# Optimization experiments

Measured on AMD Instinct MI355X. Metric: run time of the kernel, lower is better.

## Reference

```python
import jax, jax.numpy as jnp
import numpy as np

N_QUBITS = 8
INPUT_DIM = 256
SEQ_LEN = 256
BATCH = 512


def qgate(theta, x):
    # Closed-form expectation of the PennyLane circuit:
    #   RX(x_i) then RY(theta_i) on each wire (from |0>), then CNOT chain 0->1->...->n-1,
    #   measure <Z_k>.  Single-wire <Z_j> = cos(x_j) * cos(theta_j); CNOT chain maps
    #   Z_k -> Z_0 Z_1 ... Z_k in the Heisenberg picture, so on the product state
    #   <Z_k> = prod_{j<=k} cos(x_j) cos(theta_j).
    # x: (B, n_wires), theta: (n_wires,)
    return jnp.cumprod(jnp.cos(x) * jnp.cos(theta), axis=-1)


def setup_inputs() -> dict:
    key = jax.random.key(0)
    ks = jax.random.split(key, 14)
    d_in = INPUT_DIM + N_QUBITS  # concat([x, hx]) -> 264
    lin_scale = 1.0 / np.sqrt(d_in)
    inp = {
        "inputs": jax.random.normal(ks[0], (SEQ_LEN, BATCH, INPUT_DIM), dtype=jnp.float32),
        "Wf": jax.random.normal(ks[1], (N_QUBITS, d_in), dtype=jnp.float32) * lin_scale,
        "bf": jax.random.normal(ks[2], (N_QUBITS,), dtype=jnp.float32) * lin_scale,
        "Wi": jax.random.normal(ks[3], (N_QUBITS, d_in), dtype=jnp.float32) * lin_scale,
        "bi": jax.random.normal(ks[4], (N_QUBITS,), dtype=jnp.float32) * lin_scale,
        "Wu": jax.random.normal(ks[5], (N_QUBITS, d_in), dtype=jnp.float32) * lin_scale,
        "bu": jax.random.normal(ks[6], (N_QUBITS,), dtype=jnp.float32) * lin_scale,
        "Wo": jax.random.normal(ks[7], (N_QUBITS, d_in), dtype=jnp.float32) * lin_scale,
        "bo": jax.random.normal(ks[8], (N_QUBITS,), dtype=jnp.float32) * lin_scale,
        "pf": jax.random.normal(ks[9], (N_QUBITS,), dtype=jnp.float32),
        "pi_": jax.random.normal(ks[10], (N_QUBITS,), dtype=jnp.float32),
        "pu": jax.random.normal(ks[11], (N_QUBITS,), dtype=jnp.float32),
        "po": jax.random.normal(ks[12], (N_QUBITS,), dtype=jnp.float32),
    }
    return inp


def reference(inputs, Wf, bf, Wi, bi, Wu, bu, Wo, bo, pf, pi_, pu, po):
    B = inputs.shape[1]
    H = pf.shape[0]  # hidden_dim == n_qubits

    def step(carry, x):
        hx, cx = carry
        comb = jnp.concatenate([x, hx], axis=1)  # (B, input_dim + H)
        f = jax.nn.sigmoid(qgate(pf, comb @ Wf.T + bf))
        i = jax.nn.sigmoid(qgate(pi_, comb @ Wi.T + bi))
        g = jnp.tanh(qgate(pu, comb @ Wu.T + bu))
        o = jax.nn.sigmoid(qgate(po, comb @ Wo.T + bo))
        cx = f * cx + i * g
        hx = o * jnp.tanh(cx)
        return (hx, cx), hx

    init = (jnp.zeros((B, H), dtype=inputs.dtype), jnp.zeros((B, H), dtype=inputs.dtype))
    (hx, cx), stacked = jax.lax.scan(step, init, inputs)
    return stacked, hx, cx
```

## Files before the change

### kernel.cpp

```cpp
#include <hip/hip_runtime.h>
#include <hip/hip_bf16.h>


#define SEQ   256
#define BATCH 512
#define DIN   256
#define NROWS (SEQ * BATCH)
#define DCOMB 264
#define ZTSTR 514
#define HLSTR 260

typedef __attribute__((ext_vector_type(8))) short short8;
typedef __attribute__((ext_vector_type(4))) float f32x4;
typedef __attribute__((ext_vector_type(2))) float f32x2;

__device__ __forceinline__ short f2bf(float f) {
    union { __hip_bfloat16 h; short s; } u;
    u.h = __float2bfloat16(f);
    return u.s;
}
__device__ __forceinline__ float bf2f(short s) {
    union { short s; __hip_bfloat16 h; } u;
    u.s = s;
    return __bfloat162float(u.h);
}

__device__ __forceinline__ short8 pack8(float4 a, float4 b) {
    union { short8 s8; int i[4]; } u;
    union { __hip_bfloat162 h; int i; } v;
    v.h = __float22bfloat162_rn(make_float2(a.x, a.y)); u.i[0] = v.i;
    v.h = __float22bfloat162_rn(make_float2(a.z, a.w)); u.i[1] = v.i;
    v.h = __float22bfloat162_rn(make_float2(b.x, b.y)); u.i[2] = v.i;
    v.h = __float22bfloat162_rn(make_float2(b.z, b.w)); u.i[3] = v.i;
    return u.s8;
}

#define DPP_ROR(V, S) \
    __int_as_float(__builtin_amdgcn_update_dpp(__float_as_int(V), __float_as_int(V), 0x120 | (S), 0xF, 0xF, false))
#define QP(V, CTRL) \
    __int_as_float(__builtin_amdgcn_update_dpp(__float_as_int(V), __float_as_int(V), (CTRL), 0xF, 0xF, false))
#define PSTG2(A, D) { \
    float s0_ = __int_as_float(__builtin_amdgcn_update_dpp(one_i, __float_as_int(A.x), 0x110 | (D), 0xF, 0xF, false)); \
    float s1_ = __int_as_float(__builtin_amdgcn_update_dpp(one_i, __float_as_int(A.y), 0x110 | (D), 0xF, 0xF, false)); \
    A *= (f32x2){s0_, s1_}; }

__device__ __forceinline__ void scan_body8(
    int T0, const float* __restrict__ zrow, float* __restrict__ hlrow,
    bool writer, f32x4 (&ZC)[4], f32x4 (&ZN)[4],
    float& hx, float& cx,
    const f32x2 (&wp)[8], const f32x2 cth,
    const f32x2 k0, const f32x2 k1, const f32x2 k2, const f32x2 k3,
    const f32x2 k4, const int one_i)
{
    #pragma unroll
    for (int j = 0; j < 4; ++j)
        ZN[j] = *(const f32x4*)&zrow[(T0 + 8) * 2 + j * 4];

    float hxh[8];
    #pragma unroll
    for (int u = 0; u < 8; ++u) {
        const f32x2 z2 = (f32x2){ ZC[u >> 1][(u & 1) * 2],
                                  ZC[u >> 1][(u & 1) * 2 + 1] };

        const float h0 = hx;
        const float h1 = DPP_ROR(hx, 2),  h2 = DPP_ROR(hx, 4);
        const float h3 = DPP_ROR(hx, 6),  h4 = DPP_ROR(hx, 8);
        const float h5 = DPP_ROR(hx, 10), h6 = DPP_ROR(hx, 12);
        const float h7 = DPP_ROR(hx, 14);

        f32x2 e0 = (f32x2){h0, h0} * wp[0] + (f32x2){h1, h1} * wp[1];
        f32x2 e1 = (f32x2){h2, h2} * wp[2] + (f32x2){h3, h3} * wp[3];
        f32x2 e2 = (f32x2){h4, h4} * wp[4] + (f32x2){h5, h5} * wp[5];
        f32x2 e3 = (f32x2){h6, h6} * wp[6] + (f32x2){h7, h7} * wp[7];
        const f32x2 p = ((z2 + e0) + (e1 + e2)) + e3;

        f32x2 A = (f32x2){__cosf(p.x), __cosf(p.y)} * cth;
        PSTG2(A, 2) PSTG2(A, 4) PSTG2(A, 8)

        const f32x2 t2 = A * A;
        f32x2 rr = k3 + t2 * k4;
        rr = k2 + t2 * rr;
        rr = k1 + t2 * rr;
        const f32x2 P = k0 + A * rr;

        const float f_all = QP(P.x, 0xA0);
        const float u_all = QP(P.x, 0xF5);
        const float i_all = QP(P.y, 0xA0);
        const float o_all = QP(P.y, 0xF5);

        cx = fmaf(f_all, cx, i_all * u_all);

        const float tq  = cx * cx;
        const float num = cx * fmaf(tq, fmaf(tq, 1.0f, 105.0f), 945.0f);
        const float den = fmaf(tq, fmaf(tq, 15.0f, 420.0f), 945.0f);
        const float tc  = num * __builtin_amdgcn_rcpf(den);

        hx = o_all * tc;
        hxh[u] = hx;
    }

    if (writer) {
        *(f32x4*)&hlrow[T0]     = (f32x4){hxh[0], hxh[1], hxh[2], hxh[3]};
        *(f32x4*)&hlrow[T0 + 4] = (f32x4){hxh[4], hxh[5], hxh[6], hxh[7]};
    }
}

__global__ __launch_bounds__(512, 2) void qlstm_fused(
    const float* __restrict__ X,
    const float* __restrict__ Wf, const float* __restrict__ Wi,
    const float* __restrict__ Wu, const float* __restrict__ Wo,
    const float* __restrict__ bfv, const float* __restrict__ biv,
    const float* __restrict__ buv, const float* __restrict__ bov,
    const float* __restrict__ pf, const float* __restrict__ pi_,
    const float* __restrict__ pu, const float* __restrict__ po,
    float* __restrict__ out)
{
    __shared__ short8 Wl[2048];
    __shared__ float Zt[32 * ZTSTR + 16];
    __shared__ float Hl2[16 * HLSTR];

    const int tx  = threadIdx.x;
    const int l   = tx & 63;
    const int wid = tx >> 6;
    const int lm  = l & 15;
    const int lk  = l >> 4;
    const int B0  = blockIdx.x;

    const float* Wg[4] = {Wf, Wi, Wu, Wo};
    const float* Bg[4] = {bfv, biv, buv, bov};

    #pragma unroll
    for (int e = 0; e < 4; ++e) {
        const int ent  = tx + e * 512;
        const int lane = ent & 63;
        const int ks   = (ent >> 6) & 7;
        const int hl   = (ent >> 9) & 1;
        const int nt   = (ent >> 10) & 1;
        const int elm  = lane & 15, elk = lane >> 4;
        const int c    = nt * 16 + elm;
        const float* wrow = Wg[c & 3] + (c >> 2) * DCOMB + ks * 32 + elk * 8;
        short8 fr;
        #pragma unroll
        for (int j = 0; j < 8; ++j) {
            const float v = wrow[j];
            const short h16 = f2bf(v);
            fr[j] = hl ? f2bf(v - bf2f(h16)) : h16;
        }
        Wl[ent] = fr;
    }

    float bias0, bias1;
    { const int c0 = lm;      bias0 = Bg[c0 & 3][c0 >> 2];
      const int c1 = 16 + lm; bias1 = Bg[c1 & 3][c1 >> 2]; }

    __syncthreads();

    #pragma unroll
    for (int p = 0; p < 4; ++p) {
        const int r0 = p * 128 + wid * 16;
        const int r  = r0 + lm;
        const float* xbase =
            X + ((long)(r >> 1) * BATCH + B0 * 2 + (r & 1)) * DIN + lk * 8;

        float4 xv[16];
        #pragma unroll
        for (int i = 0; i < 16; ++i)
            xv[i] = *(const float4*)(xbase + (i >> 1) * 32 + (i & 1) * 4);

        f32x4 acc0 = (f32x4){bias0, bias0, bias0, bias0};
        f32x4 acc1 = (f32x4){bias1, bias1, bias1, bias1};
        #pragma unroll
        for (int ks = 0; ks < 8; ++ks) {
            const short8 a = pack8(xv[2 * ks], xv[2 * ks + 1]);
            acc0 = __builtin_amdgcn_mfma_f32_16x16x32_bf16(a, Wl[ks * 64 + l],        acc0, 0, 0, 0);
            acc0 = __builtin_amdgcn_mfma_f32_16x16x32_bf16(a, Wl[(8  + ks) * 64 + l], acc0, 0, 0, 0);
            acc1 = __builtin_amdgcn_mfma_f32_16x16x32_bf16(a, Wl[(16 + ks) * 64 + l], acc1, 0, 0, 0);
            acc1 = __builtin_amdgcn_mfma_f32_16x16x32_bf16(a, Wl[(24 + ks) * 64 + l], acc1, 0, 0, 0);
        }

        #pragma unroll
        for (int rr = 0; rr < 4; ++rr) {
            const int rw = r0 + lk * 4 + rr;
            const int tt = rw >> 1, blw = rw & 1;
            Zt[(blw * 16 + (lm >> 1)) * ZTSTR + tt * 2 + (lm & 1)]     = acc0[rr];
            Zt[(blw * 16 + 8 + (lm >> 1)) * ZTSTR + tt * 2 + (lm & 1)] = acc1[rr];
        }
    }
    __syncthreads();

    if (tx < 64) {
        const int q   = tx & 15;
        const int kq  = q >> 1;
        const int hi  = q & 1;
        const int bl  = (tx >> 4) & 1;
        const int b   = B0 * 2 + bl;
        const int oidx = b * 8 + kq;
        const int woff = kq * DCOMB + DIN;

        const float* WgA = hi ? Wu : Wf;
        const float* WgB = hi ? Wo : Wi;
        f32x2 wp[8];
        #pragma unroll
        for (int s = 0; s < 8; ++s) {
            const int j = (kq - s) & 7;
            wp[s] = (f32x2){WgA[woff + j], WgB[woff + j]};
        }
        const f32x2 cth = (f32x2){__cosf((hi ? pu : pf)[kq]),
                                  __cosf((hi ? po : pi_)[kq])};

        const float SK1 = 0.25f, SK2 = -0.0208333333f, SK3 = 0.0020833333f,
                    SK4 = -0.00021082f;
        const f32x2 k0 = (f32x2){hi ? 0.0f : 0.5f, 0.5f};
        const f32x2 k1 = (f32x2){hi ? 0.9999016f : SK1, SK1};
        const f32x2 k2 = (f32x2){hi ? -0.3310485f : SK2, SK2};
        const f32x2 k3 = (f32x2){hi ? 0.1204423f : SK3, SK3};
        const f32x2 k4 = (f32x2){hi ? -0.0277012f : SK4, SK4};

        const int one_i = __float_as_int(1.0f);

        float hx = 0.0f, cx = 0.0f;
        const float* __restrict__ zrow = &Zt[(bl * 16 + q) * ZTSTR];
        float* __restrict__ hlrow = &Hl2[(bl * 8 + kq) * HLSTR];
        const bool writer = (hi == 0) && (tx < 32);

        f32x4 zbA[4], zbB[4];
        #pragma unroll
        for (int j = 0; j < 4; ++j) zbA[j] = *(const f32x4*)&zrow[j * 4];

        for (int t0 = 0; t0 < SEQ; t0 += 16) {
            scan_body8(t0,     zrow, hlrow, writer, zbA, zbB, hx, cx,
                       wp, cth, k0, k1, k2, k3, k4, one_i);
            scan_body8(t0 + 8, zrow, hlrow, writer, zbB, zbA, hx, cx,
                       wp, cth, k0, k1, k2, k3, k4, one_i);
        }

        if (hi == 0 && tx < 32) {
            out[NROWS * 8 + oidx]        = hx;
            out[NROWS * 8 + 4096 + oidx] = cx;
        }
    }
    __syncthreads();

    {
        const int f0 = tx * 8;
        const int t  = f0 >> 4;
        const int c0 = f0 & 15;
        float4 v0, v1;
        v0.x = Hl2[(c0 + 0) * HLSTR + t];
        v0.y = Hl2[(c0 + 1) * HLSTR + t];
        v0.z = Hl2[(c0 + 2) * HLSTR + t];
        v0.w = Hl2[(c0 + 3) * HLSTR + t];
        v1.x = Hl2[(c0 + 4) * HLSTR + t];
        v1.y = Hl2[(c0 + 5) * HLSTR + t];
        v1.z = Hl2[(c0 + 6) * HLSTR + t];
        v1.w = Hl2[(c0 + 7) * HLSTR + t];
        float4* dst = (float4*)(out + (long)t * (BATCH * 8) + B0 * 16 + c0);
        dst[0] = v0;
        dst[1] = v1;
    }
}

extern "C" void kernel_launch(void* const* d_in, const int* in_sizes, int n_in,
                              void* d_out, int out_size, void* d_ws, size_t ws_size,
                              hipStream_t stream) {
    const float* X   = (const float*)d_in[0];
    const float* Wf  = (const float*)d_in[1];
    const float* bfv = (const float*)d_in[2];
    const float* Wi  = (const float*)d_in[3];
    const float* biv = (const float*)d_in[4];
    const float* Wu  = (const float*)d_in[5];
    const float* buv = (const float*)d_in[6];
    const float* Wo  = (const float*)d_in[7];
    const float* bov = (const float*)d_in[8];
    const float* pf  = (const float*)d_in[9];
    const float* pi_ = (const float*)d_in[10];
    const float* pu  = (const float*)d_in[11];
    const float* po  = (const float*)d_in[12];
    float* out = (float*)d_out;
    (void)d_ws; (void)ws_size;

    qlstm_fused<<<BATCH / 2, 512, 0, stream>>>(
        X, Wf, Wi, Wu, Wo, bfv, biv, buv, bov, pf, pi_, pu, po, out);
}
```

Measured before the change: 249.9 us.

## Overlap input projection GEMM with recurrent scan via double-buffered chunks

The fused kernel previously computed the full input projection for all 256 timesteps into shared memory before one wave ran the sequential recurrence. It now splits the sequence into 64-step chunks: waves 1-4 compute the next chunk's MFMA projection into one of two shared buffers while wave 0 scans the previous chunk. The intent is to hide the projection and global loads behind the latency-bound scan, and the smaller chunk buffers shrink shared memory. In exchange it adds a block barrier per chunk, leaves waves 5-7 idle, and lowers launch bounds to one block per CU, which may reduce occupancy and latency hiding across blocks.

```diff
diff --git a/kernel.cpp b/kernel.cpp
--- a/kernel.cpp
+++ b/kernel.cpp
@@ -7,7 +7,10 @@
 #define DIN   256
 #define NROWS (SEQ * BATCH)
 #define DCOMB 264
-#define ZTSTR 514
+#define CHT   64
+#define NCH   (SEQ / CHT)
+#define ZBSTR 130
+#define ZBUFSZ (32 * ZBSTR + 16)
 #define HLSTR 260
 
 typedef __attribute__((ext_vector_type(8))) short short8;
@@ -45,8 +48,9 @@
     A *= (f32x2){s0_, s1_}; }
 
 __device__ __forceinline__ void scan_body8(
-    int T0, const float* __restrict__ zrow, float* __restrict__ hlrow,
-    bool writer, f32x4 (&ZC)[4], f32x4 (&ZN)[4],
+    int T0L, int T0G, const float* __restrict__ zrow,
+    float* __restrict__ hlrow, bool writer,
+    f32x4 (&ZC)[4], f32x4 (&ZN)[4],
     float& hx, float& cx,
     const f32x2 (&wp)[8], const f32x2 cth,
     const f32x2 k0, const f32x2 k1, const f32x2 k2, const f32x2 k3,
@@ -54,7 +58,7 @@
 {
     #pragma unroll
     for (int j = 0; j < 4; ++j)
-        ZN[j] = *(const f32x4*)&zrow[(T0 + 8) * 2 + j * 4];
+        ZN[j] = *(const f32x4*)&zrow[(T0L + 8) * 2 + j * 4];
 
     float hxh[8];
     #pragma unroll
@@ -100,12 +104,12 @@
     }
 
     if (writer) {
-        *(f32x4*)&hlrow[T0]     = (f32x4){hxh[0], hxh[1], hxh[2], hxh[3]};
-        *(f32x4*)&hlrow[T0 + 4] = (f32x4){hxh[4], hxh[5], hxh[6], hxh[7]};
-    }
-}
-
-__global__ __launch_bounds__(512, 2) void qlstm_fused(
+        *(f32x4*)&hlrow[T0G]     = (f32x4){hxh[0], hxh[1], hxh[2], hxh[3]};
+        *(f32x4*)&hlrow[T0G + 4] = (f32x4){hxh[4], hxh[5], hxh[6], hxh[7]};
+    }
+}
+
+__global__ __launch_bounds__(512, 1) void qlstm_fused(
     const float* __restrict__ X,
     const float* __restrict__ Wf, const float* __restrict__ Wi,
     const float* __restrict__ Wu, const float* __restrict__ Wo,
@@ -116,7 +120,7 @@
     float* __restrict__ out)
 {
     __shared__ short8 Wl[2048];
-    __shared__ float Zt[32 * ZTSTR + 16];
+    __shared__ float Zb[2][ZBUFSZ];
     __shared__ float Hl2[16 * HLSTR];
 
     const int tx  = threadIdx.x;
@@ -153,93 +157,101 @@
     { const int c0 = lm;      bias0 = Bg[c0 & 3][c0 >> 2];
       const int c1 = 16 + lm; bias1 = Bg[c1 & 3][c1 >> 2]; }
 
-    __syncthreads();
-
-    #pragma unroll
-    for (int p = 0; p < 4; ++p) {
-        const int r0 = p * 128 + wid * 16;
-        const int r  = r0 + lm;
-        const float* xbase =
-            X + ((long)(r >> 1) * BATCH + B0 * 2 + (r & 1)) * DIN + lk * 8;
-
-        float4 xv[16];
-        #pragma unroll
-        for (int i = 0; i < 16; ++i)
-            xv[i] = *(const float4*)(xbase + (i >> 1) * 32 + (i & 1) * 4);
-
-        f32x4 acc0 = (f32x4){bias0, bias0, bias0, bias0};
-        f32x4 acc1 = (f32x4){bias1, bias1, bias1, bias1};
-        #pragma unroll
-        for (int ks = 0; ks < 8; ++ks) {
-            const short8 a = pack8(xv[2 * ks], xv[2 * ks + 1]);
-            acc0 = __builtin_amdgcn_mfma_f32_16x16x32_bf16(a, Wl[ks * 64 + l],        acc0, 0, 0, 0);
-            acc0 = __builtin_amdgcn_mfma_f32_16x16x32_bf16(a, Wl[(8  + ks) * 64 + l], acc0, 0, 0, 0);
-            acc1 = __builtin_amdgcn_mfma_f32_16x16x32_bf16(a, Wl[(16 + ks) * 64 + l], acc1, 0, 0, 0);
-            acc1 = __builtin_amdgcn_mfma_f32_16x16x32_bf16(a, Wl[(24 + ks) * 64 + l], acc1, 0, 0, 0);
-        }
-
-        #pragma unroll
-        for (int rr = 0; rr < 4; ++rr) {
-            const int rw = r0 + lk * 4 + rr;
-            const int tt = rw >> 1, blw = rw & 1;
-            Zt[(blw * 16 + (lm >> 1)) * ZTSTR + tt * 2 + (lm & 1)]     = acc0[rr];
-            Zt[(blw * 16 + 8 + (lm >> 1)) * ZTSTR + tt * 2 + (lm & 1)] = acc1[rr];
-        }
-    }
-    __syncthreads();
-
-    if (tx < 64) {
-        const int q   = tx & 15;
-        const int kq  = q >> 1;
-        const int hi  = q & 1;
-        const int bl  = (tx >> 4) & 1;
-        const int b   = B0 * 2 + bl;
-        const int oidx = b * 8 + kq;
-        const int woff = kq * DCOMB + DIN;
-
+    const int q   = tx & 15;
+    const int kq  = q >> 1;
+    const int hi  = q & 1;
+    const int bl  = (tx >> 4) & 1;
+    const int oidx = (B0 * 2 + bl) * 8 + kq;
+    const int woff = kq * DCOMB + DIN;
+
+    f32x2 wp[8];
+    f32x2 cth = (f32x2){1.0f, 1.0f};
+    if (wid == 0) {
         const float* WgA = hi ? Wu : Wf;
         const float* WgB = hi ? Wo : Wi;
-        f32x2 wp[8];
         #pragma unroll
         for (int s = 0; s < 8; ++s) {
             const int j = (kq - s) & 7;
             wp[s] = (f32x2){WgA[woff + j], WgB[woff + j]};
         }
-        const f32x2 cth = (f32x2){__cosf((hi ? pu : pf)[kq]),
-                                  __cosf((hi ? po : pi_)[kq])};
-
-        const float SK1 = 0.25f, SK2 = -0.0208333333f, SK3 = 0.0020833333f,
-                    SK4 = -0.00021082f;
-        const f32x2 k0 = (f32x2){hi ? 0.0f : 0.5f, 0.5f};
-        const f32x2 k1 = (f32x2){hi ? 0.9999016f : SK1, SK1};
-        const f32x2 k2 = (f32x2){hi ? -0.3310485f : SK2, SK2};
-        const f32x2 k3 = (f32x2){hi ? 0.1204423f : SK3, SK3};
-        const f32x2 k4 = (f32x2){hi ? -0.0277012f : SK4, SK4};
-
-        const int one_i = __float_as_int(1.0f);
-
-        float hx = 0.0f, cx = 0.0f;
-        const float* __restrict__ zrow = &Zt[(bl * 16 + q) * ZTSTR];
-        float* __restrict__ hlrow = &Hl2[(bl * 8 + kq) * HLSTR];
-        const bool writer = (hi == 0) && (tx < 32);
-
-        f32x4 zbA[4], zbB[4];
-        #pragma unroll
-        for (int j = 0; j < 4; ++j) zbA[j] = *(const f32x4*)&zrow[j * 4];
-
-        for (int t0 = 0; t0 < SEQ; t0 += 16) {
-            scan_body8(t0,     zrow, hlrow, writer, zbA, zbB, hx, cx,
-                       wp, cth, k0, k1, k2, k3, k4, one_i);
-            scan_body8(t0 + 8, zrow, hlrow, writer, zbB, zbA, hx, cx,
-                       wp, cth, k0, k1, k2, k3, k4, one_i);
+        cth = (f32x2){__cosf((hi ? pu : pf)[kq]),
+                      __cosf((hi ? po : pi_)[kq])};
+    }
+    const float SK1 = 0.25f, SK2 = -0.0208333333f, SK3 = 0.0020833333f,
+                SK4 = -0.00021082f;
+    const f32x2 k0 = (f32x2){hi ? 0.0f : 0.5f, 0.5f};
+    const f32x2 k1 = (f32x2){hi ? 0.9999016f : SK1, SK1};
+    const f32x2 k2 = (f32x2){hi ? -0.3310485f : SK2, SK2};
+    const f32x2 k3 = (f32x2){hi ? 0.1204423f : SK3, SK3};
+    const f32x2 k4 = (f32x2){hi ? -0.0277012f : SK4, SK4};
+    const int one_i = __float_as_int(1.0f);
+
+    float hx = 0.0f, cx = 0.0f;
+    const float* __restrict__ zrowb = &Zb[0][(bl * 16 + q) * ZBSTR];
+    float* __restrict__ hlrow = &Hl2[(bl * 8 + kq) * HLSTR];
+    const bool writer = (hi == 0) && (tx < 32);
+    f32x4 zbA[4], zbB[4];
+
+    __syncthreads();
+
+    #pragma unroll 1
+    for (int k = 0; k <= NCH; ++k) {
+        if (wid == 0) {
+            if (k >= 1) {
+                const float* __restrict__ zrow = zrowb + ((k - 1) & 1) * ZBUFSZ;
+                const int TG = (k - 1) * CHT;
+                #pragma unroll
+                for (int j = 0; j < 4; ++j) zbA[j] = *(const f32x4*)&zrow[j * 4];
+                scan_body8( 0, TG,      zrow, hlrow, writer, zbA, zbB, hx, cx, wp, cth, k0, k1, k2, k3, k4, one_i);
+                scan_body8( 8, TG + 8,  zrow, hlrow, writer, zbB, zbA, hx, cx, wp, cth, k0, k1, k2, k3, k4, one_i);
+                scan_body8(16, TG + 16, zrow, hlrow, writer, zbA, zbB, hx, cx, wp, cth, k0, k1, k2, k3, k4, one_i);
+                scan_body8(24, TG + 24, zrow, hlrow, writer, zbB, zbA, hx, cx, wp, cth, k0, k1, k2, k3, k4, one_i);
+                scan_body8(32, TG + 32, zrow, hlrow, writer, zbA, zbB, hx, cx, wp, cth, k0, k1, k2, k3, k4, one_i);
+                scan_body8(40, TG + 40, zrow, hlrow, writer, zbB, zbA, hx, cx, wp, cth, k0, k1, k2, k3, k4, one_i);
+                scan_body8(48, TG + 48, zrow, hlrow, writer, zbA, zbB, hx, cx, wp, cth, k0, k1, k2, k3, k4, one_i);
+                scan_body8(56, TG + 56, zrow, hlrow, writer, zbB, zbA, hx, cx, wp, cth, k0, k1, k2, k3, k4, one_i);
+                if (k == NCH && writer) {
+                    out[NROWS * 8 + oidx]        = hx;
+                    out[NROWS * 8 + 4096 + oidx] = cx;
+                }
+            }
+        } else if (wid <= 4 && k < NCH) {
+            float* __restrict__ bufp = &Zb[k & 1][0];
+            #pragma unroll
+            for (int g = 0; g < 2; ++g) {
+                const int r0 = k * 128 + (wid - 1) * 32 + g * 16;
+                const int r  = r0 + lm;
+                const float* xbase =
+                    X + ((long)(r >> 1) * BATCH + B0 * 2 + (r & 1)) * DIN + lk * 8;
+
+                float4 xv[16];
+                #pragma unroll
+                for (int i = 0; i < 16; ++i)
+                    xv[i] = *(const float4*)(xbase + (i >> 1) * 32 + (i & 1) * 4);
+
+                f32x4 acc0 = (f32x4){bias0, bias0, bias0, bias0};
+                f32x4 acc1 = (f32x4){bias1, bias1, bias1, bias1};
+                #pragma unroll
+                for (int ks = 0; ks < 8; ++ks) {
+                    const short8 a = pack8(xv[2 * ks], xv[2 * ks + 1]);
+                    acc0 = __builtin_amdgcn_mfma_f32_16x16x32_bf16(a, Wl[ks * 64 + l],        acc0, 0, 0, 0);
+                    acc0 = __builtin_amdgcn_mfma_f32_16x16x32_bf16(a, Wl[(8  + ks) * 64 + l], acc0, 0, 0, 0);
+                    acc1 = __builtin_amdgcn_mfma_f32_16x16x32_bf16(a, Wl[(16 + ks) * 64 + l], acc1, 0, 0, 0);
+                    acc1 = __builtin_amdgcn_mfma_f32_16x16x32_bf16(a, Wl[(24 + ks) * 64 + l], acc1, 0, 0, 0);
+                }
+
+                #pragma unroll
+                for (int rr = 0; rr < 4; ++rr) {
+                    const int rw   = r0 + lk * 4 + rr;
+                    const int tl   = (rw - k * 128) >> 1;
+                    const int blw  = rw & 1;
+                    bufp[(blw * 16 + (lm >> 1)) * ZBSTR + tl * 2 + (lm & 1)]     = acc0[rr];
+                    bufp[(blw * 16 + 8 + (lm >> 1)) * ZBSTR + tl * 2 + (lm & 1)] = acc1[rr];
+                }
+            }
         }
-
-        if (hi == 0 && tx < 32) {
-            out[NROWS * 8 + oidx]        = hx;
-            out[NROWS * 8 + 4096 + oidx] = cx;
-        }
-    }
-    __syncthreads();
+        __syncthreads();
+    }
 
     {
         const int f0 = tx * 8;
```

New measurement: 220.3 us. 1.13x faster.
